# Optimization experiments

Hardware: AMD Instinct MI355X
Metric: run time of the kernel (lower is better)

Reference implementation:

```python
import jax, jax.numpy as jnp
import numpy as np

NUM_GROUPS = 32
EPS = 1e-6


def group_norm(x, gamma, beta):
    # x: [B, C, H, W]
    B, C, H, W = x.shape
    xg = x.reshape(B, NUM_GROUPS, C // NUM_GROUPS, H, W)
    mu = jnp.mean(xg, axis=(2, 3, 4), keepdims=True)
    var = jnp.var(xg, axis=(2, 3, 4), keepdims=True)
    xg = (xg - mu) * jax.lax.rsqrt(var + EPS)
    x = xg.reshape(B, C, H, W)
    return x * gamma[None, :, None, None] + beta[None, :, None, None]


def conv1x1(x, w, b):
    # x: [B, C, H, W], w: [O, C], b: [O]
    return jnp.einsum('bchw,oc->bohw', x, w) + b[None, :, None, None]


def setup_inputs() -> dict:
    key = jax.random.key(0)
    C = 512
    B, H, W = 4, 64, 64
    ks = jax.random.split(key, 10)
    s = 1.0 / np.sqrt(C)
    inp = {
        'x': jax.random.normal(ks[0], (B, C, H, W), dtype=jnp.float32),
        'gamma': jnp.ones((C,), dtype=jnp.float32),
        'beta': jnp.zeros((C,), dtype=jnp.float32),
        'wq': jax.random.normal(ks[1], (C, C), dtype=jnp.float32) * s,
        'bq': jnp.zeros((C,), dtype=jnp.float32),
        'wk': jax.random.normal(ks[2], (C, C), dtype=jnp.float32) * s,
        'bk': jnp.zeros((C,), dtype=jnp.float32),
        'wv': jax.random.normal(ks[3], (C, C), dtype=jnp.float32) * s,
        'bv': jnp.zeros((C,), dtype=jnp.float32),
        'wo': jax.random.normal(ks[4], (C, C), dtype=jnp.float32) * s,
        'bo': jnp.zeros((C,), dtype=jnp.float32),
    }
    return inp


def reference(x, gamma, beta, wq, bq, wk, bk, wv, bv, wo, bo):
    B, C, H, W = x.shape
    h = group_norm(x, gamma, beta)
    q = conv1x1(h, wq, bq).reshape(B, C, H * W)  # [B, C, S]
    k = conv1x1(h, wk, bk).reshape(B, C, H * W)
    v = conv1x1(h, wv, bv).reshape(B, C, H * W)
    scale = C ** (-0.5)
    # scores[b, S, s] = sum_c q[b, c, S] * k[b, c, s]
    w = jnp.einsum('bcS,bcs->bSs', q, k) * scale
    w = jax.nn.softmax(w, axis=-1)
    # out[b, c, S] = sum_s w[b, S, s] * v[b, c, s]
    hattn = jnp.einsum('bSs,bcs->bcS', w, v).reshape(B, C, H, W)
    out = conv1x1(hattn, wo, bo)
    return x + out
```

## Files before the change

kernel.cpp:

```cpp
#include <hip/hip_runtime.h>

#define B_   4
#define C_   512
#define S_   4096
#define G_   32
#define CPG_ 16
#define EPS_ 1e-6f

typedef unsigned short u16;
typedef __bf16 bf16x8 __attribute__((ext_vector_type(8)));
typedef float  f32x4  __attribute__((ext_vector_type(4)));

__device__ __forceinline__ u16 f2bf(float f) {
  unsigned u = __float_as_uint(f);
  u += 0x7fffu + ((u >> 16) & 1u);
  return (u16)(u >> 16);
}
__device__ __forceinline__ float bf2f(u16 h) {
  return __uint_as_float((unsigned)h << 16);
}

__device__ __forceinline__ void g2lds16(const void* g, void* l) {
  __builtin_amdgcn_global_load_lds(
      (const __attribute__((address_space(1))) void*)g,
      (__attribute__((address_space(3))) void*)l, 16, 0, 0);
}

#define BAR()    __builtin_amdgcn_s_barrier()
#define SCHED0() __builtin_amdgcn_sched_barrier(0)
#define WAITV4   asm volatile("s_waitcnt vmcnt(4)" ::: "memory")
#define WAITV0   asm volatile("s_waitcnt vmcnt(0)" ::: "memory")
#define LGKM0    asm volatile("s_waitcnt lgkmcnt(0)" ::: "memory")

__device__ __forceinline__ void xcd_swz(int& bx, int& by, int& bz) {
  const int gx = gridDim.x, gy = gridDim.y;
  const int nwg = gx * gy * (int)gridDim.z;
  const int flat = blockIdx.x + gx * (blockIdx.y + gy * blockIdx.z);
  const int q = nwg >> 3;
  const int nf = (flat & 7) * q + (flat >> 3);
  bx = nf % gx;
  const int r = nf / gx;
  by = r % gy;
  bz = r / gy;
}

__global__ __launch_bounds__(256) void f32_to_bf16(const float* __restrict__ in,
                                                   u16* __restrict__ out, int n) {
  int i = blockIdx.x * 256 + threadIdx.x;
  if (i < n) out[i] = f2bf(in[i]);
}

__global__ __launch_bounds__(256) void concat_bias(const float* __restrict__ a,
                                                   const float* __restrict__ b,
                                                   float* __restrict__ o) {
  int i = blockIdx.x * 256 + threadIdx.x;
  o[i] = (i < 512) ? a[i] : b[i - 512];
}

__global__ __launch_bounds__(256) void add_bf16(const u16* __restrict__ a,
                                                const u16* __restrict__ b,
                                                u16* __restrict__ o) {
  const int i = blockIdx.x * 256 + threadIdx.x;
  const uint4 ua = ((const uint4*)a)[i];
  const uint4 ub = ((const uint4*)b)[i];
  const unsigned* pa = (const unsigned*)&ua;
  const unsigned* pb = (const unsigned*)&ub;
  unsigned r[4];
#pragma unroll
  for (int k = 0; k < 4; ++k) {
    const float lo = bf2f((u16)(pa[k] & 0xffffu)) + bf2f((u16)(pb[k] & 0xffffu));
    const float hi = bf2f((u16)(pa[k] >> 16)) + bf2f((u16)(pb[k] >> 16));
    r[k] = (unsigned)f2bf(lo) | ((unsigned)f2bf(hi) << 16);
  }
  ((uint4*)o)[i] = *(const uint4*)r;
}

__global__ __launch_bounds__(256) void gn_stats(const float* __restrict__ x,
                                                float* __restrict__ stats) {
  const int bg = blockIdx.x;
  const float4* p4 = (const float4*)(x + (size_t)bg * (CPG_ * S_));
  float s = 0.f, ss = 0.f;
  const int tid = threadIdx.x;
  for (int i = tid; i < CPG_ * S_ / 4; i += 256) {
    float4 v = p4[i];
    s  += v.x + v.y + v.z + v.w;
    ss += v.x * v.x + v.y * v.y + v.z * v.z + v.w * v.w;
  }
#pragma unroll
  for (int o = 32; o; o >>= 1) { s += __shfl_xor(s, o, 64); ss += __shfl_xor(ss, o, 64); }
  __shared__ float sm[8];
  const int wid = tid >> 6, lane = tid & 63;
  if (lane == 0) { sm[wid * 2] = s; sm[wid * 2 + 1] = ss; }
  __syncthreads();
  if (tid == 0) {
    s  = sm[0] + sm[2] + sm[4] + sm[6];
    ss = sm[1] + sm[3] + sm[5] + sm[7];
    const float inv = 1.f / (float)(CPG_ * S_);
    float mu = s * inv;
    float var = ss * inv - mu * mu;
    stats[bg * 2]     = mu;
    stats[bg * 2 + 1] = rsqrtf(var + EPS_);
  }
}

__global__ __launch_bounds__(256) void gn_apply_t(const float* __restrict__ x,
                                                  const float* __restrict__ gamma,
                                                  const float* __restrict__ beta,
                                                  const float* __restrict__ stats,
                                                  u16* __restrict__ ht) {
  __shared__ float tile[32][33];
  const int b = blockIdx.z, c0 = blockIdx.y * 32, s0 = blockIdx.x * 32;
  const int tx = threadIdx.x, ty = threadIdx.y;
#pragma unroll
  for (int i = 0; i < 4; ++i) {
    const int c  = c0 + ty + i * 8;
    const float mu = stats[(b * G_ + (c >> 4)) * 2];
    const float rs = stats[(b * G_ + (c >> 4)) * 2 + 1];
    const float v  = x[((size_t)b * C_ + c) * S_ + s0 + tx];
    tile[ty + i * 8][tx] = (v - mu) * rs * gamma[c] + beta[c];
  }
  __syncthreads();
#pragma unroll
  for (int i = 0; i < 4; ++i) {
    const int s = s0 + ty + i * 8;
    ht[((size_t)b * S_ + s) * C_ + c0 + tx] = f2bf(tile[tx][ty + i * 8]);
  }
}

template <int BIAS_MODE, int ZMODE>
__global__ __launch_bounds__(512, 2) void gemm8p(
    const u16* __restrict__ Ag, int lda, long sA,
    const u16* __restrict__ Bg, int ldb, long sB,
    u16* __restrict__ Cg, int ldc, long sC,
    const float* __restrict__ bias, float alpha, int K) {
  __shared__ u16 As[2][2][8192];
  __shared__ u16 Bs[2][2][8192];
  int bx, by, bz;
  xcd_swz(bx, by, bz);
  const u16 *A, *Bm;
  u16* Cb;
  if (ZMODE == 0) {
    A = Ag + (size_t)bz * sA; Bm = Bg + (size_t)bz * sB; Cb = Cg + (size_t)bz * sC;
  } else {
    const int b = bz >> 1, kh = bz & 1;
    A  = Ag + (size_t)b * 16777216 + (size_t)kh * 2048;
    Bm = Bg + (size_t)b * 4096 + (size_t)kh * 2048;
    Cb = Cg + (size_t)kh * 8388608 + (size_t)b * 2097152;
  }
  const int bm = by * 256, bn = bx * 256;
  const int tid = threadIdx.x;
  const int wid = tid >> 6, lane = tid & 63;
  const int wm = (wid >> 2) * 16, wn = (wid & 3) * 16;
  const int lr = lane & 15, lh = lane >> 4;
  const int x7 = lr & 7;
  const int g0 = (lh ^ x7) * 8, g1 = ((4 | lh) ^ x7) * 8;

  const int sg = (lane & 7) ^ ((lane >> 3) & 7);
  const u16* Abase = A  + (size_t)(bm + wid * 8 + (lane >> 3)) * lda + sg * 8;
  const u16* Bbase = Bm + (size_t)(bn + wid * 8 + (lane >> 3)) * ldb + sg * 8;

#define STGA(D, H, T) do {                                                   \
    const u16* _s = Abase + (size_t)((H) * 128) * lda + (size_t)(T) * 64;    \
    g2lds16(_s,                    &As[D][H][wid * 512]);                    \
    g2lds16(_s + (size_t)64 * lda, &As[D][H][4096 + wid * 512]);             \
  } while (0)
#define STGB(D, H, T) do {                                                   \
    const u16* _s = Bbase + (size_t)((H) * 128) * ldb + (size_t)(T) * 64;    \
    g2lds16(_s,                    &Bs[D][H][wid * 512]);                    \
    g2lds16(_s + (size_t)64 * ldb, &Bs[D][H][4096 + wid * 512]);             \
  } while (0)

  float bias_v[4] = {0.f, 0.f, 0.f, 0.f};
  if (BIAS_MODE == 1) {
#pragma unroll
    for (int g = 0; g < 4; ++g) bias_v[g] = bias[bn + wn + g * 64 + lr];
  }
  SCHED0();

  f32x4 acc[8][4];
  const f32x4 zero = {0.f, 0.f, 0.f, 0.f};
#pragma unroll
  for (int i = 0; i < 8; ++i)
#pragma unroll
    for (int j = 0; j < 4; ++j) acc[i][j] = zero;

  bf16x8 a_[4][2], b_[4][2];

#define RDA(D, AH) do {                                                      \
    _Pragma("unroll") for (int i = 0; i < 4; ++i) {                          \
      const int _o = (wm + i * 32 + lr) * 64;                                \
      a_[i][0] = *(const bf16x8*)&As[D][AH][_o + g0];                        \
      a_[i][1] = *(const bf16x8*)&As[D][AH][_o + g1];                        \
    } } while (0)
#define RDBALL(D) do {                                                       \
    _Pragma("unroll") for (int j = 0; j < 4; ++j) {                          \
      const int _o = (wn + (j & 1) * 64 + lr) * 64;                          \
      b_[j][0] = *(const bf16x8*)&Bs[D][j >> 1][_o + g0];                    \
      b_[j][1] = *(const bf16x8*)&Bs[D][j >> 1][_o + g1];                    \
    } } while (0)
#define MM(AH, BH) do {                                                      \
    __builtin_amdgcn_s_setprio(1);                                           \
    _Pragma("unroll") for (int i = 0; i < 4; ++i)                            \
    _Pragma("unroll") for (int j = 0; j < 2; ++j) {                          \
      acc[(AH) * 4 + i][(BH) * 2 + j] = __builtin_amdgcn_mfma_f32_16x16x32_bf16( \
          a_[i][0], b_[(BH) * 2 + j][0], acc[(AH) * 4 + i][(BH) * 2 + j], 0, 0, 0); \
      acc[(AH) * 4 + i][(BH) * 2 + j] = __builtin_amdgcn_mfma_f32_16x16x32_bf16( \
          a_[i][1], b_[(BH) * 2 + j][1], acc[(AH) * 4 + i][(BH) * 2 + j], 0, 0, 0); \
    }                                                                        \
    __builtin_amdgcn_s_setprio(0);                                           \
  } while (0)
#define MID() SCHED0(); BAR(); LGKM0; SCHED0()

  STGA(0, 0, 0); STGB(0, 1, 0); STGA(0, 1, 0); STGB(0, 0, 0);
  STGA(1, 0, 1); STGB(1, 1, 1);
  WAITV4;
  BAR();

  const int nt = K >> 6;
  for (int i = 0; i < nt / 2; ++i) {
    const int t1 = 2 * i + 1, t2 = 2 * i + 2, t3 = 2 * i + 3;
    const bool s2 = t2 < nt, s3 = t3 < nt;
    RDA(0, 0); RDBALL(0);
    STGB(1, 0, t1);
    MID(); MM(0, 0); BAR();
    STGA(1, 1, t1);
    MID(); MM(0, 1); BAR();
    RDA(0, 1);
    if (s2) STGA(0, 0, t2);
    MID(); MM(1, 1); BAR();
    if (s2) STGB(0, 1, t2);
    MID(); MM(1, 0);
    if (s2) { WAITV4; } else { WAITV0; }
    BAR();
    RDA(1, 0); RDBALL(1);
    if (s2) STGA(0, 1, t2);
    MID(); MM(0, 0); BAR();
    if (s2) STGB(0, 0, t2);
    MID(); MM(0, 1); BAR();
    RDA(1, 1);
    if (s3) STGA(1, 0, t3);
    MID(); MM(1, 1); BAR();
    if (s3) STGB(1, 1, t3);
    MID(); MM(1, 0);
    if (s3) { WAITV4; }
    BAR();
  }
#undef STGA
#undef STGB
#undef RDA
#undef RDBALL
#undef MM
#undef MID
  SCHED0();

#pragma unroll
  for (int f = 0; f < 8; ++f) {
    const int row0 = bm + wm + f * 32 + lh * 4;
#pragma unroll
    for (int g = 0; g < 4; ++g) {
      const int col = bn + wn + g * 64 + lr;
#pragma unroll
      for (int r = 0; r < 4; ++r)
        Cb[(size_t)(row0 + r) * ldc + col] = f2bf(acc[f][g][r] * alpha + bias_v[g]);
    }
  }
}

#define GBM 128
#define GBN 128
#define GBK 64

template <int BIAS_MODE, int OUT_MODE>
__global__ __launch_bounds__(256) void gemm_abT(
    const u16* __restrict__ Ag, int lda, long sA,
    const u16* __restrict__ Bg, int ldb, long sB,
    void* __restrict__ Cg, int ldc, long sC,
    const float* __restrict__ bias, float alpha,
    const float* __restrict__ xres, int K) {
  __shared__ u16 As[GBM * GBK];
  __shared__ u16 Bs[GBN * GBK];
  const int bz = blockIdx.z;
  const u16* A    = Ag + (size_t)bz * sA;
  const u16* Bmat = Bg + (size_t)bz * sB;
  const int bm = blockIdx.y * GBM, bn = blockIdx.x * GBN;
  const int tid = threadIdx.x;
  const int wid = tid >> 6, lane = tid & 63;
  const int wm = (wid >> 1) * 64, wn = (wid & 1) * 64;
  const int lr = lane & 15, lh = lane >> 4;
  const int srow = lane >> 3, scol = (lane & 7) * 8;

  f32x4 acc[4][4];
  const f32x4 zero = {0.f, 0.f, 0.f, 0.f};
#pragma unroll
  for (int i = 0; i < 4; ++i)
#pragma unroll
    for (int j = 0; j < 4; ++j) acc[i][j] = zero;

  for (int k0 = 0; k0 < K; k0 += GBK) {
    __syncthreads();
#pragma unroll
    for (int i = 0; i < 4; ++i) {
      const int chunk = wid * 4 + i;
      const int row   = chunk * 8 + srow;
      g2lds16(A    + (size_t)(bm + row) * lda + (k0 + scol), &As[chunk * 512]);
      g2lds16(Bmat + (size_t)(bn + row) * ldb + (k0 + scol), &Bs[chunk * 512]);
    }
    __syncthreads();
#pragma unroll
    for (int ks = 0; ks < 2; ++ks) {
      bf16x8 a_[4], b_[4];
#pragma unroll
      for (int m = 0; m < 4; ++m)
        a_[m] = *(const bf16x8*)&As[(wm + m * 16 + lr) * GBK + ks * 32 + lh * 8];
#pragma unroll
      for (int n = 0; n < 4; ++n)
        b_[n] = *(const bf16x8*)&Bs[(wn + n * 16 + lr) * GBK + ks * 32 + lh * 8];
#pragma unroll
      for (int m = 0; m < 4; ++m)
#pragma unroll
        for (int n = 0; n < 4; ++n)
          acc[m][n] = __builtin_amdgcn_mfma_f32_16x16x32_bf16(a_[m], b_[n], acc[m][n], 0, 0, 0);
    }
  }

  if (OUT_MODE == 0) {
    u16* Cb = (u16*)Cg + (size_t)bz * sC;
#pragma unroll
    for (int m = 0; m < 4; ++m) {
      const int row0 = bm + wm + m * 16 + lh * 4;
#pragma unroll
      for (int n = 0; n < 4; ++n) {
        const int col = bn + wn + n * 16 + lr;
        float bn_ = (BIAS_MODE == 1) ? bias[col] : 0.f;
#pragma unroll
        for (int r = 0; r < 4; ++r) {
          float bb = (BIAS_MODE == 2) ? bias[row0 + r] : bn_;
          Cb[(size_t)(row0 + r) * ldc + col] = f2bf(acc[m][n][r] * alpha + bb);
        }
      }
    }
  } else {
    float* Ob = (float*)Cg;
#pragma unroll
    for (int m = 0; m < 4; ++m) {
      const int row0 = bm + wm + m * 16 + lh * 4;
#pragma unroll
      for (int n = 0; n < 4; ++n) {
        const int col = bn + wn + n * 16 + lr;
        const int bb = col >> 12, sp = col & (S_ - 1);
#pragma unroll
        for (int r = 0; r < 4; ++r) {
          const int o = row0 + r;
          const size_t idx = ((size_t)bb * C_ + o) * S_ + sp;
          Ob[idx] = acc[m][n][r] * alpha + bias[o] + xres[idx];
        }
      }
    }
  }
}

__global__ __launch_bounds__(256) void softmax_rows(u16* __restrict__ sc) {
  const size_t base = ((size_t)blockIdx.y * S_ + blockIdx.x) * S_;
  uint4* r4 = (uint4*)(sc + base);
  const int tid = threadIdx.x;
  uint4 u0 = r4[tid], u1 = r4[tid + 256];
  float f[16];
  {
    const unsigned* pu = (const unsigned*)&u0;
    const unsigned* pv = (const unsigned*)&u1;
#pragma unroll
    for (int i = 0; i < 4; ++i) {
      f[2 * i]     = bf2f((u16)(pu[i] & 0xffffu));
      f[2 * i + 1] = bf2f((u16)(pu[i] >> 16));
      f[8 + 2 * i]     = bf2f((u16)(pv[i] & 0xffffu));
      f[8 + 2 * i + 1] = bf2f((u16)(pv[i] >> 16));
    }
  }
  float mx = f[0];
#pragma unroll
  for (int i = 1; i < 16; ++i) mx = fmaxf(mx, f[i]);
#pragma unroll
  for (int o = 32; o; o >>= 1) mx = fmaxf(mx, __shfl_xor(mx, o, 64));
  __shared__ float red[8];
  const int wid = tid >> 6, lane = tid & 63;
  if (lane == 0) red[wid] = mx;
  __syncthreads();
  mx = fmaxf(fmaxf(red[0], red[1]), fmaxf(red[2], red[3]));
  float s = 0.f;
#pragma unroll
  for (int i = 0; i < 16; ++i) { f[i] = __expf(f[i] - mx); s += f[i]; }
#pragma unroll
  for (int o = 32; o; o >>= 1) s += __shfl_xor(s, o, 64);
  if (lane == 0) red[4 + wid] = s;
  __syncthreads();
  s = red[4] + red[5] + red[6] + red[7];
  const float inv = 1.f / s;
  unsigned o0[4], o1[4];
#pragma unroll
  for (int i = 0; i < 4; ++i) {
    o0[i] = (unsigned)f2bf(f[2 * i] * inv)     | ((unsigned)f2bf(f[2 * i + 1] * inv) << 16);
    o1[i] = (unsigned)f2bf(f[8 + 2 * i] * inv) | ((unsigned)f2bf(f[8 + 2 * i + 1] * inv) << 16);
  }
  r4[tid]       = *(uint4*)o0;
  r4[tid + 256] = *(uint4*)o1;
}

extern "C" void kernel_launch(void* const* d_in, const int* in_sizes, int n_in,
                              void* d_out, int out_size, void* d_ws, size_t ws_size,
                              hipStream_t stream) {
  const float* x     = (const float*)d_in[0];
  const float* gamma = (const float*)d_in[1];
  const float* beta  = (const float*)d_in[2];
  const float* wq = (const float*)d_in[3];
  const float* bq = (const float*)d_in[4];
  const float* wk = (const float*)d_in[5];
  const float* bk = (const float*)d_in[6];
  const float* wv = (const float*)d_in[7];
  const float* bv = (const float*)d_in[8];
  const float* wo = (const float*)d_in[9];
  const float* bo = (const float*)d_in[10];
  float* out = (float*)d_out;

  char* ws = (char*)d_ws;
  float* stats = (float*)ws;
  u16* wqb = (u16*)(ws + 1024);
  u16* wkb = wqb + 262144;
  u16* wvb = wkb + 262144;
  u16* wob = wvb + 262144;
  float* bqk = (float*)(wob + 262144);
  u16* ht  = (u16*)((char*)bqk + 4096);
  u16* qkt = ht + 8388608;
  u16* vv  = qkt + 16777216;
  u16* sc  = vv + 8388608;

  f32_to_bf16<<<1024, 256, 0, stream>>>(wq, wqb, 262144);
  f32_to_bf16<<<1024, 256, 0, stream>>>(wk, wkb, 262144);
  f32_to_bf16<<<1024, 256, 0, stream>>>(wv, wvb, 262144);
  f32_to_bf16<<<1024, 256, 0, stream>>>(wo, wob, 262144);
  concat_bias<<<4, 256, 0, stream>>>(bq, bk, bqk);

  gn_stats<<<128, 256, 0, stream>>>(x, stats);
  gn_apply_t<<<dim3(128, 16, 4), dim3(32, 8), 0, stream>>>(x, gamma, beta, stats, ht);

  gemm8p<1, 0><<<dim3(4, 64, 1), 512, 0, stream>>>(ht, 512, 0, wqb, 512, 0,
                                                   qkt, 1024, 0, bqk, 1.f, 512);
  gemm_abT<2, 0><<<dim3(128, 4, 1), 256, 0, stream>>>(wvb, 512, 0, ht, 512, 0,
                                                      vv, 16384, 0, bv, 1.f, nullptr, 512);
  gemm8p<0, 0><<<dim3(16, 16, 4), 512, 0, stream>>>(qkt, 1024, 4194304, qkt + 512, 1024, 4194304,
                                                    sc, 4096, 16777216, nullptr,
                                                    0.04419417382415922f, 512);
  softmax_rows<<<dim3(4096, 4), 256, 0, stream>>>(sc);
  gemm8p<0, 1><<<dim3(2, 16, 8), 512, 0, stream>>>(sc, 4096, 0, vv, 16384, 0,
                                                   qkt, 512, 0, nullptr, 1.f, 2048);
  add_bf16<<<4096, 256, 0, stream>>>(qkt, qkt + 8388608, vv);
  gemm_abT<2, 1><<<dim3(128, 4, 1), 256, 0, stream>>>(wob, 512, 0, vv, 512, 0,
                                                      out, 0, 0, bo, 1.f, x, 512);
}
```

Measured before the change: 318.7 us.

## Fuse softmax exponent and row-sum partials into QK^T GEMM epilogue

Drops the separate softmax kernel. The score GEMM epilogue now writes exp(score*scale) as bf16 and emits per-tile row-sum partials; a small kernel reduces those partials into reciprocals, and the scale by 1/sum is applied in the bf16 add after the PV GEMM. This removes a full read-and-write pass over the large score matrix. It gives up max subtraction, so it depends on scores staying small enough not to overflow in exp. B-fragment LDS reads are also split into halves and interleaved with the MFMA phases.

```diff
diff --git a/kernel.cpp b/kernel.cpp
--- a/kernel.cpp
+++ b/kernel.cpp
@@ -57,10 +57,25 @@
   o[i] = (i < 512) ? a[i] : b[i - 512];
 }
 
-__global__ __launch_bounds__(256) void add_bf16(const u16* __restrict__ a,
-                                                const u16* __restrict__ b,
-                                                u16* __restrict__ o) {
+__global__ __launch_bounds__(256) void reduce_l(const float* __restrict__ p,
+                                                float* __restrict__ lr) {
   const int i = blockIdx.x * 256 + threadIdx.x;
+  const int b = i >> 12, row = i & 4095;
+  float s = 0.f;
+#pragma unroll
+  for (int jb = 0; jb < 16; ++jb) s += p[((size_t)(b * 16 + jb) << 12) + row];
+  lr[i] = 1.f / s;
+}
+
+__global__ __launch_bounds__(256) void add_scale_bf16(const u16* __restrict__ a,
+                                                      const u16* __restrict__ b,
+                                                      const float* __restrict__ lr,
+                                                      u16* __restrict__ o) {
+  const int i = blockIdx.x * 256 + threadIdx.x;
+  const size_t i8 = (size_t)i * 8;
+  const int bi = (int)(i8 >> 21);
+  const int row = (int)(i8 >> 9) & 4095;
+  const float sc = lr[bi * 4096 + row];
   const uint4 ua = ((const uint4*)a)[i];
   const uint4 ub = ((const uint4*)b)[i];
   const unsigned* pa = (const unsigned*)&ua;
@@ -68,8 +83,8 @@
   unsigned r[4];
 #pragma unroll
   for (int k = 0; k < 4; ++k) {
-    const float lo = bf2f((u16)(pa[k] & 0xffffu)) + bf2f((u16)(pb[k] & 0xffffu));
-    const float hi = bf2f((u16)(pa[k] >> 16)) + bf2f((u16)(pb[k] >> 16));
+    const float lo = (bf2f((u16)(pa[k] & 0xffffu)) + bf2f((u16)(pb[k] & 0xffffu))) * sc;
+    const float hi = (bf2f((u16)(pa[k] >> 16)) + bf2f((u16)(pb[k] >> 16))) * sc;
     r[k] = (unsigned)f2bf(lo) | ((unsigned)f2bf(hi) << 16);
   }
   ((uint4*)o)[i] = *(const uint4*)r;
@@ -127,14 +142,16 @@
   }
 }
 
-template <int BIAS_MODE, int ZMODE>
+template <int BIAS_MODE, int ZMODE, int SMAX>
 __global__ __launch_bounds__(512, 2) void gemm8p(
     const u16* __restrict__ Ag, int lda, long sA,
     const u16* __restrict__ Bg, int ldb, long sB,
     u16* __restrict__ Cg, int ldc, long sC,
-    const float* __restrict__ bias, float alpha, int K) {
+    const float* __restrict__ bias, float alpha, int K,
+    float* __restrict__ smx) {
   __shared__ u16 As[2][2][8192];
   __shared__ u16 Bs[2][2][8192];
+  __shared__ float ps[4][256];
   int bx, by, bz;
   xcd_swz(bx, by, bz);
   const u16 *A, *Bm;
@@ -192,11 +209,11 @@
       a_[i][0] = *(const bf16x8*)&As[D][AH][_o + g0];                        \
       a_[i][1] = *(const bf16x8*)&As[D][AH][_o + g1];                        \
     } } while (0)
-#define RDBALL(D) do {                                                       \
-    _Pragma("unroll") for (int j = 0; j < 4; ++j) {                          \
-      const int _o = (wn + (j & 1) * 64 + lr) * 64;                          \
-      b_[j][0] = *(const bf16x8*)&Bs[D][j >> 1][_o + g0];                    \
-      b_[j][1] = *(const bf16x8*)&Bs[D][j >> 1][_o + g1];                    \
+#define RDB(D, BH) do {                                                      \
+    _Pragma("unroll") for (int j = 0; j < 2; ++j) {                          \
+      const int _o = (wn + j * 64 + lr) * 64;                                \
+      b_[(BH) * 2 + j][0] = *(const bf16x8*)&Bs[D][BH][_o + g0];             \
+      b_[(BH) * 2 + j][1] = *(const bf16x8*)&Bs[D][BH][_o + g1];             \
     } } while (0)
 #define MM(AH, BH) do {                                                      \
     __builtin_amdgcn_s_setprio(1);                                           \
@@ -220,9 +237,10 @@
   for (int i = 0; i < nt / 2; ++i) {
     const int t1 = 2 * i + 1, t2 = 2 * i + 2, t3 = 2 * i + 3;
     const bool s2 = t2 < nt, s3 = t3 < nt;
-    RDA(0, 0); RDBALL(0);
+    RDA(0, 0); RDB(0, 0);
     STGB(1, 0, t1);
     MID(); MM(0, 0); BAR();
+    RDB(0, 1);
     STGA(1, 1, t1);
     MID(); MM(0, 1); BAR();
     RDA(0, 1);
@@ -232,9 +250,10 @@
     MID(); MM(1, 0);
     if (s2) { WAITV4; } else { WAITV0; }
     BAR();
-    RDA(1, 0); RDBALL(1);
+    RDA(1, 0); RDB(1, 0);
     if (s2) STGA(0, 1, t2);
     MID(); MM(0, 0); BAR();
+    RDB(1, 1);
     if (s2) STGB(0, 0, t2);
     MID(); MM(0, 1); BAR();
     RDA(1, 1);
@@ -248,20 +267,60 @@
 #undef STGA
 #undef STGB
 #undef RDA
-#undef RDBALL
+#undef RDB
 #undef MM
 #undef MID
   SCHED0();
 
-#pragma unroll
-  for (int f = 0; f < 8; ++f) {
-    const int row0 = bm + wm + f * 32 + lh * 4;
-#pragma unroll
-    for (int g = 0; g < 4; ++g) {
-      const int col = bn + wn + g * 64 + lr;
+  if (SMAX) {
+    float rs[8][4];
+#pragma unroll
+    for (int f = 0; f < 8; ++f) {
+      const int row0 = bm + wm + f * 32 + lh * 4;
+#pragma unroll
+      for (int r = 0; r < 4; ++r) rs[f][r] = 0.f;
+#pragma unroll
+      for (int g = 0; g < 4; ++g) {
+        const int col = bn + wn + g * 64 + lr;
+#pragma unroll
+        for (int r = 0; r < 4; ++r) {
+          const float e = __expf(acc[f][g][r] * alpha);
+          rs[f][r] += e;
+          Cb[(size_t)(row0 + r) * ldc + col] = f2bf(e);
+        }
+      }
+#pragma unroll
+      for (int r = 0; r < 4; ++r) {
+        float v = rs[f][r];
+        v += __shfl_xor(v, 1, 64);
+        v += __shfl_xor(v, 2, 64);
+        v += __shfl_xor(v, 4, 64);
+        v += __shfl_xor(v, 8, 64);
+        rs[f][r] = v;
+      }
+    }
+#pragma unroll
+    for (int f = 0; f < 8; ++f)
 #pragma unroll
       for (int r = 0; r < 4; ++r)
-        Cb[(size_t)(row0 + r) * ldc + col] = f2bf(acc[f][g][r] * alpha + bias_v[g]);
+        if (lr == ((f << 1) | (r >> 1)))
+          ps[wid & 3][wm + f * 32 + lh * 4 + r] = rs[f][r];
+    __syncthreads();
+    if (tid < 256) {
+      const float tot = ps[0][tid] + ps[1][tid] + ps[2][tid] + ps[3][tid];
+      smx[((size_t)(bz * 16 + bx) << 12) + bm + tid] = tot;
+    }
+  } else {
+#pragma unroll
+    for (int f = 0; f < 8; ++f) {
+      const int row0 = bm + wm + f * 32 + lh * 4;
+#pragma unroll
+      for (int g = 0; g < 4; ++g) {
+        const int col = bn + wn + g * 64 + lr;
+#pragma unroll
+        for (int r = 0; r < 4; ++r)
+          Cb[(size_t)(row0 + r) * ldc + col] = f2bf(acc[f][g][r] * alpha + bias_v[g]);
+      }
     }
   }
 }
@@ -359,52 +418,6 @@
   }
 }
 
-__global__ __launch_bounds__(256) void softmax_rows(u16* __restrict__ sc) {
-  const size_t base = ((size_t)blockIdx.y * S_ + blockIdx.x) * S_;
-  uint4* r4 = (uint4*)(sc + base);
-  const int tid = threadIdx.x;
-  uint4 u0 = r4[tid], u1 = r4[tid + 256];
-  float f[16];
-  {
-    const unsigned* pu = (const unsigned*)&u0;
-    const unsigned* pv = (const unsigned*)&u1;
-#pragma unroll
-    for (int i = 0; i < 4; ++i) {
-      f[2 * i]     = bf2f((u16)(pu[i] & 0xffffu));
-      f[2 * i + 1] = bf2f((u16)(pu[i] >> 16));
-      f[8 + 2 * i]     = bf2f((u16)(pv[i] & 0xffffu));
-      f[8 + 2 * i + 1] = bf2f((u16)(pv[i] >> 16));
-    }
-  }
-  float mx = f[0];
-#pragma unroll
-  for (int i = 1; i < 16; ++i) mx = fmaxf(mx, f[i]);
-#pragma unroll
-  for (int o = 32; o; o >>= 1) mx = fmaxf(mx, __shfl_xor(mx, o, 64));
-  __shared__ float red[8];
-  const int wid = tid >> 6, lane = tid & 63;
-  if (lane == 0) red[wid] = mx;
-  __syncthreads();
-  mx = fmaxf(fmaxf(red[0], red[1]), fmaxf(red[2], red[3]));
-  float s = 0.f;
-#pragma unroll
-  for (int i = 0; i < 16; ++i) { f[i] = __expf(f[i] - mx); s += f[i]; }
-#pragma unroll
-  for (int o = 32; o; o >>= 1) s += __shfl_xor(s, o, 64);
-  if (lane == 0) red[4 + wid] = s;
-  __syncthreads();
-  s = red[4] + red[5] + red[6] + red[7];
-  const float inv = 1.f / s;
-  unsigned o0[4], o1[4];
-#pragma unroll
-  for (int i = 0; i < 4; ++i) {
-    o0[i] = (unsigned)f2bf(f[2 * i] * inv)     | ((unsigned)f2bf(f[2 * i + 1] * inv) << 16);
-    o1[i] = (unsigned)f2bf(f[8 + 2 * i] * inv) | ((unsigned)f2bf(f[8 + 2 * i + 1] * inv) << 16);
-  }
-  r4[tid]       = *(uint4*)o0;
-  r4[tid + 256] = *(uint4*)o1;
-}
-
 extern "C" void kernel_launch(void* const* d_in, const int* in_sizes, int n_in,
                               void* d_out, int out_size, void* d_ws, size_t ws_size,
                               hipStream_t stream) {
@@ -432,6 +445,8 @@
   u16* qkt = ht + 8388608;
   u16* vv  = qkt + 16777216;
   u16* sc  = vv + 8388608;
+  float* partials = (float*)(sc + 67108864);
+  float* Lr = partials + 262144;
 
   f32_to_bf16<<<1024, 256, 0, stream>>>(wq, wqb, 262144);
   f32_to_bf16<<<1024, 256, 0, stream>>>(wk, wkb, 262144);
@@ -442,17 +457,17 @@
   gn_stats<<<128, 256, 0, stream>>>(x, stats);
   gn_apply_t<<<dim3(128, 16, 4), dim3(32, 8), 0, stream>>>(x, gamma, beta, stats, ht);
 
-  gemm8p<1, 0><<<dim3(4, 64, 1), 512, 0, stream>>>(ht, 512, 0, wqb, 512, 0,
-                                                   qkt, 1024, 0, bqk, 1.f, 512);
+  gemm8p<1, 0, 0><<<dim3(4, 64, 1), 512, 0, stream>>>(ht, 512, 0, wqb, 512, 0,
+                                                      qkt, 1024, 0, bqk, 1.f, 512, nullptr);
   gemm_abT<2, 0><<<dim3(128, 4, 1), 256, 0, stream>>>(wvb, 512, 0, ht, 512, 0,
                                                       vv, 16384, 0, bv, 1.f, nullptr, 512);
-  gemm8p<0, 0><<<dim3(16, 16, 4), 512, 0, stream>>>(qkt, 1024, 4194304, qkt + 512, 1024, 4194304,
-                                                    sc, 4096, 16777216, nullptr,
-                                                    0.04419417382415922f, 512);
-  softmax_rows<<<dim3(4096, 4), 256, 0, stream>>>(sc);
-  gemm8p<0, 1><<<dim3(2, 16, 8), 512, 0, stream>>>(sc, 4096, 0, vv, 16384, 0,
-                                                   qkt, 512, 0, nullptr, 1.f, 2048);
-  add_bf16<<<4096, 256, 0, stream>>>(qkt, qkt + 8388608, vv);
+  gemm8p<0, 0, 1><<<dim3(16, 16, 4), 512, 0, stream>>>(qkt, 1024, 4194304, qkt + 512, 1024, 4194304,
+                                                       sc, 4096, 16777216, nullptr,
+                                                       0.04419417382415922f, 512, partials);
+  reduce_l<<<64, 256, 0, stream>>>(partials, Lr);
+  gemm8p<0, 1, 0><<<dim3(2, 16, 8), 512, 0, stream>>>(sc, 4096, 0, vv, 16384, 0,
+                                                      qkt, 512, 0, nullptr, 1.f, 2048, nullptr);
+  add_scale_bf16<<<4096, 256, 0, stream>>>(qkt, qkt + 8388608, Lr, vv);
   gemm_abT<2, 1><<<dim3(128, 4, 1), 256, 0, stream>>>(wob, 512, 0, vv, 512, 0,
                                                       out, 0, 0, bo, 1.f, x, 512);
 }
```

Measured after the change: 293.8 us. 1.08x faster.
